# Optimization experiments

Hardware: AMD Instinct MI355X
Metric: run time of the kernel (lower is better)

## Reference

```python
import jax, jax.numpy as jnp
import numpy as np

H = 128
NH = 8  # num attention heads


def _ln(x, g, b, eps=1e-5):
    m = x.mean(-1, keepdims=True)
    v = ((x - m) ** 2).mean(-1, keepdims=True)
    return (x - m) / jnp.sqrt(v + eps) * g + b


def _mha(q_in, kv_in, Wqkv, bqkv, Wo, bo):
    # torch nn.MultiheadAttention with packed in_proj, batch=1, eval (no dropout)
    h = q_in.shape[-1]
    hd = h // NH
    Wq, Wk, Wv = Wqkv[:h], Wqkv[h:2 * h], Wqkv[2 * h:]
    bq, bk, bv = bqkv[:h], bqkv[h:2 * h], bqkv[2 * h:]
    q = (q_in @ Wq.T + bq).reshape(-1, NH, hd).transpose(1, 0, 2)   # [nh, Nq, hd]
    k = (kv_in @ Wk.T + bk).reshape(-1, NH, hd).transpose(1, 0, 2)  # [nh, Nk, hd]
    v = (kv_in @ Wv.T + bv).reshape(-1, NH, hd).transpose(1, 0, 2)
    scores = jnp.einsum('hqd,hkd->hqk', q, k) / jnp.sqrt(jnp.asarray(hd, q.dtype))
    attn = jax.nn.softmax(scores, axis=-1)
    out = jnp.einsum('hqk,hkd->hqd', attn, v)                       # [nh, Nq, hd]
    out = out.transpose(1, 0, 2).reshape(-1, h)
    return out @ Wo.T + bo


def setup_inputs() -> dict:
    key = jax.random.key(0)
    ks = jax.random.split(key, 32)
    s = 0.05
    d = {
        'ligand_features': jax.random.normal(ks[0], (512, 128), jnp.float32),
        'pocket_features': jax.random.normal(ks[1], (1024, 128), jnp.float32),
        'ligand_coords': jax.random.uniform(ks[2], (512, 3), jnp.float32) * 20.0,
        'pocket_coords': jax.random.uniform(ks[3], (1024, 3), jnp.float32) * 20.0,
        # projections
        'Wl': jax.random.normal(ks[4], (H, 128), jnp.float32) * s,
        'bl': jnp.zeros((H,), jnp.float32),
        'Wp': jax.random.normal(ks[5], (H, 128), jnp.float32) * s,
        'bp': jnp.zeros((H,), jnp.float32),
        # distance encoder: 1 -> h/4 -> h/2 -> h
        'Wd1': jax.random.normal(ks[6], (H // 4, 1), jnp.float32) * s,
        'bd1': jnp.zeros((H // 4,), jnp.float32),
        'Wd2': jax.random.normal(ks[7], (H // 2, H // 4), jnp.float32) * s,
        'bd2': jnp.zeros((H // 2,), jnp.float32),
        'Wd3': jax.random.normal(ks[8], (H, H // 2), jnp.float32) * s,
        'bd3': jnp.zeros((H,), jnp.float32),
        # gates
        'Wgl': jax.random.normal(ks[9], (H, 2 * H), jnp.float32) * s,
        'bgl': jnp.zeros((H,), jnp.float32),
        'Wgp': jax.random.normal(ks[10], (H, 2 * H), jnp.float32) * s,
        'bgp': jnp.zeros((H,), jnp.float32),
        # shared cross-attention (packed qkv like torch)
        'Wqkv': jax.random.normal(ks[11], (3 * H, H), jnp.float32) * s,
        'bqkv': jnp.zeros((3 * H,), jnp.float32),
        'Wo': jax.random.normal(ks[12], (H, H), jnp.float32) * s,
        'bo': jnp.zeros((H,), jnp.float32),
        # layer norms
        'g_l': jnp.ones((H,), jnp.float32),
        'be_l': jnp.zeros((H,), jnp.float32),
        'g_p': jnp.ones((H,), jnp.float32),
        'be_p': jnp.zeros((H,), jnp.float32),
    }
    return d


def reference(ligand_features, pocket_features, ligand_coords, pocket_coords,
              Wl, bl, Wp, bp, Wd1, bd1, Wd2, bd2, Wd3, bd3,
              Wgl, bgl, Wgp, bgp, Wqkv, bqkv, Wo, bo,
              g_l, be_l, g_p, be_p):
    lig = ligand_features @ Wl.T + bl   # [Nl, H]
    poc = pocket_features @ Wp.T + bp   # [Np, H]

    # pairwise distances [Nl, Np]
    diff = ligand_coords[:, None, :] - pocket_coords[None, :, :]
    dist = jnp.sqrt(jnp.sum(diff * diff, axis=-1))

    # distance encoder MLP applied elementwise -> [Nl, Np, H]
    e = jax.nn.relu(dist[..., None] @ Wd1.T + bd1)
    e = jax.nn.relu(e @ Wd2.T + bd2)
    enc = e @ Wd3.T + bd3
    m = enc.mean(axis=-1)               # [Nl, Np]

    # ligand enhancement: softmax over pocket axis
    sw_l = jax.nn.softmax(-m, axis=-1)          # [Nl, Np]
    agg_l = sw_l @ poc                          # [Nl, H]
    gate_l = jax.nn.sigmoid(jnp.concatenate([lig, agg_l], axis=-1) @ Wgl.T + bgl)
    lig_enh = gate_l * lig + (1.0 - gate_l) * agg_l

    # pocket enhancement: transposed encoding, softmax over ligand axis
    sw_p = jax.nn.softmax(-m.T, axis=-1)        # [Np, Nl]
    agg_p = sw_p @ lig                          # [Np, H]
    gate_p = jax.nn.sigmoid(jnp.concatenate([poc, agg_p], axis=-1) @ Wgp.T + bgp)
    poc_enh = gate_p * poc + (1.0 - gate_p) * agg_p

    lig_att = _mha(lig_enh, poc_enh, Wqkv, bqkv, Wo, bo)
    poc_att = _mha(poc_enh, lig_enh, Wqkv, bqkv, Wo, bo)

    lig_fused = _ln(lig_enh + lig_att, g_l, be_l)
    poc_fused = _ln(poc_enh + poc_att, g_p, be_p)
    return (lig_fused, poc_fused)
```

## Files before the change

kernel.cpp:

```cpp
#include <hip/hip_runtime.h>
#include <hip/hip_cooperative_groups.h>
#include <math.h>

namespace cg = cooperative_groups;

#define NL 512
#define NP 1024
#define HDIM 128

#define TAB_N 8192
#define DMAX 34.65f

#define M_OFF    128
#define WLT_OFF  (M_OFF)
#define WPT_OFF  (M_OFF + 16384)
#define WQT_OFF  (M_OFF + 32768)
#define WOT_OFF  (M_OFF + 81920)
#define WGLT_OFF (M_OFF + 98304)
#define WGPT_OFF (M_OFF + 131072)
#define TAB_OFF  (M_OFF + 163840)
#define LIG_OFF  (M_OFF + NL*NP)
#define POC_OFF  (LIG_OFF + NL*HDIM)
#define LENH_OFF (POC_OFF + NP*HDIM)
#define PENH_OFF (LENH_OFF + NL*HDIM)
#define QKVL_OFF (PENH_OFF + NP*HDIM)
#define QKVP_OFF (QKVL_OFF + NL*384)
#define PARTL_OFF (QKVP_OFF + NP*384)
#define PARTP_OFF (PARTL_OFF + 512*8*8*18)

__device__ __forceinline__ float dot4f(float4 a, float4 b){
  return fmaf(a.x,b.x, fmaf(a.y,b.y, fmaf(a.z,b.z, a.w*b.w)));
}

template<int PER>
__device__ __forceinline__ void agg_task(int t, int r0,
                                         const float* __restrict__ myC,
                                         const float* __restrict__ otC,
                                         const float* __restrict__ otherFeat,
                                         const float* __restrict__ tab,
                                         float* __restrict__ smem,
                                         float* __restrict__ aggDst)
{
  const int n = PER * 256;
  float*  w     = smem;
  float4* part4 = (float4*)(smem + 4096);
  float*  redm  = smem + 6144;
  float*  sgm   = smem + 6152;
  float*  sinv  = smem + 6154;

  int rr = t >> 8, u = t & 255;
  int lane = t & 63, wv = t >> 6;
  int row = r0 + rr;
  const float inv_h = (float)(TAB_N - 1) / DMAX;

  float cx = myC[row*3+0], cy = myC[row*3+1], cz = myC[row*3+2];

  float xs[PER];
  float lmax = -1e30f;
  #pragma unroll
  for (int k = 0; k < PER; k++){
    int j = u + (k << 8);
    float ox = otC[j*3+0], oy = otC[j*3+1], oz = otC[j*3+2];
    float dx = cx-ox, dy = cy-oy, dz = cz-oz;
    float d = sqrtf(fmaf(dx,dx, fmaf(dy,dy, dz*dz)));
    float xf = d * inv_h;
    int i0 = (int)xf;
    i0 = (i0 > TAB_N-2) ? (TAB_N-2) : i0;
    float f = xf - (float)i0;
    float v0 = tab[i0], v1 = tab[i0+1];
    xs[k] = -fmaf(f, v1 - v0, v0);
    lmax = fmaxf(lmax, xs[k]);
  }
  float v = lmax;
  #pragma unroll
  for (int off = 32; off; off >>= 1) v = fmaxf(v, __shfl_down(v, off));
  if (lane == 0) redm[wv] = v;
  __syncthreads();
  if (t < 2) sgm[t] = fmaxf(fmaxf(redm[t*4+0], redm[t*4+1]), fmaxf(redm[t*4+2], redm[t*4+3]));
  __syncthreads();
  float gm = sgm[rr];
  float lsum = 0.f;
  #pragma unroll
  for (int k = 0; k < PER; k++){
    float e = __expf(xs[k] - gm);
    w[rr*n + u + (k << 8)] = e;
    lsum += e;
  }
  v = lsum;
  #pragma unroll
  for (int off = 32; off; off >>= 1) v += __shfl_down(v, off);
  if (lane == 0) redm[wv] = v;
  __syncthreads();
  if (t < 2) sinv[t] = 1.0f / ((redm[t*4+0] + redm[t*4+1]) + (redm[t*4+2] + redm[t*4+3]));
  __syncthreads();

  {
    int jg = t >> 6;
    int r  = (t >> 5) & 1;
    int c4 = t & 31;
    const int per2 = n >> 3;
    int jb0 = jg * per2;
    const float4* of4 = (const float4*)otherFeat;
    const float* wR = w + r*n;
    float4 acc = {0,0,0,0};
    #pragma unroll 4
    for (int jj = 0; jj < per2; jj++){
      int j = jb0 + jj;
      float4 f = of4[(size_t)j*32 + c4];
      float ww = wR[j];
      acc.x = fmaf(ww, f.x, acc.x); acc.y = fmaf(ww, f.y, acc.y);
      acc.z = fmaf(ww, f.z, acc.z); acc.w = fmaf(ww, f.w, acc.w);
    }
    part4[(jg*2 + r)*32 + c4] = acc;
  }
  __syncthreads();
  #pragma unroll
  for (int s2 = 4; s2 >= 1; s2 >>= 1){
    if (t < s2*64){
      int g2 = t >> 6, rem = t & 63;
      float4 a = part4[g2*64 + rem], bb = part4[(g2+s2)*64 + rem];
      a.x += bb.x; a.y += bb.y; a.z += bb.z; a.w += bb.w;
      part4[g2*64 + rem] = a;
    }
    __syncthreads();
  }
  if (t < 256) aggDst[t] = ((const float*)part4)[t] * sinv[t >> 7];
  __syncthreads();
}

__global__ __launch_bounds__(512, 2) void fused_all(
  const float* __restrict__ lf, const float* __restrict__ pf,
  const float* __restrict__ lc, const float* __restrict__ pc,
  const float* __restrict__ Wl, const float* __restrict__ bl,
  const float* __restrict__ Wp, const float* __restrict__ bp,
  const float* __restrict__ Wd1, const float* __restrict__ bd1,
  const float* __restrict__ Wd2, const float* __restrict__ bd2,
  const float* __restrict__ Wd3, const float* __restrict__ bd3,
  const float* __restrict__ Wgl, const float* __restrict__ bgl,
  const float* __restrict__ Wgp, const float* __restrict__ bgp,
  const float* __restrict__ Wqkv, const float* __restrict__ bqkv,
  const float* __restrict__ Wo, const float* __restrict__ bo,
  const float* __restrict__ g_l, const float* __restrict__ be_l,
  const float* __restrict__ g_p, const float* __restrict__ be_p,
  float* __restrict__ ws, float* __restrict__ out)
{
  cg::grid_group grd = cg::this_grid();
  const int b = blockIdx.x;
  const int t = threadIdx.x;

  __shared__ __align__(16) float smem[16384];

  float* WlT   = ws + WLT_OFF;
  float* WpT   = ws + WPT_OFF;
  float* WqkvT = ws + WQT_OFF;
  float* WoT   = ws + WOT_OFF;
  float* WglT  = ws + WGLT_OFF;
  float* WgpT  = ws + WGPT_OFF;
  float* tab   = ws + TAB_OFF;
  float* lig   = ws + LIG_OFF;
  float* poc   = ws + POC_OFF;
  float* lenh  = ws + LENH_OFF;
  float* penh  = ws + PENH_OFF;
  float* qkvl  = ws + QKVL_OFF;
  float* qkvp  = ws + QKVP_OFF;
  float* partL = ws + PARTL_OFF;
  float* partP = ws + PARTP_OFF;

  {
    int e = b*512 + t;
    if (e < 16384){
      int o = e >> 7, k = e & 127;
      WlT[k*128 + o] = Wl[e];
    } else if (e < 32768){
      int loc = e - 16384, o = loc >> 7, k = loc & 127;
      WpT[k*128 + o] = Wp[loc];
    }
    if (e < 49152){
      int o = e >> 7, k = e & 127;
      WqkvT[k*384 + o] = Wqkv[e];
    } else if (e < 65536){
      int loc = e - 49152, o = loc >> 7, k = loc & 127;
      WoT[k*128 + o] = Wo[loc];
    } else if (e < 98304){
      int loc = e - 65536, o = loc >> 8, k = loc & 255;
      WglT[k*128 + o] = Wgl[loc];
    } else {
      int loc = e - 98304, o = loc >> 8, k = loc & 255;
      WgpT[k*128 + o] = Wgp[loc];
    }

    if (b >= 240){
      float* sWd1  = smem;
      float* sbd1  = smem + 32;
      float* sbd2  = smem + 64;
      float* swd3m = smem + 128;
      float* sWd2  = smem + 256;
      if (t < 64){
        float ssum = 0.f;
        #pragma unroll 8
        for (int i = 0; i < 128; i++) ssum += Wd3[i*64 + t];
        swd3m[t] = ssum * (1.f/128.f);
      } else if (t == 64){
        float ssum = 0.f;
        for (int i = 0; i < 128; i++) ssum += bd3[i];
        smem[192] = ssum * (1.f/128.f);
      } else if (t >= 128 && t < 160){ sWd1[t-128] = Wd1[t-128]; sbd1[t-128] = bd1[t-128]; }
      else if (t >= 160 && t < 224){ sbd2[t-160] = bd2[t-160]; }
      for (int k = t; k < 2048; k += 512) sWd2[k] = Wd2[k];
      __syncthreads();

      int idx = (b - 240)*512 + t;
      float d = (float)idx * (DMAX / (float)(TAB_N - 1));
      float4 e1q[8];
      const float4* w1q = (const float4*)sWd1;
      const float4* b1q = (const float4*)sbd1;
      #pragma unroll
      for (int k4 = 0; k4 < 8; k4++){
        float4 w = w1q[k4], bb = b1q[k4];
        float4 ev;
        ev.x = fmaxf(fmaf(d, w.x, bb.x), 0.f);
        ev.y = fmaxf(fmaf(d, w.y, bb.y), 0.f);
        ev.z = fmaxf(fmaf(d, w.z, bb.z), 0.f);
        ev.w = fmaxf(fmaf(d, w.w, bb.w), 0.f);
        e1q[k4] = ev;
      }
      float mv = smem[192];
      #pragma unroll 4
      for (int j2 = 0; j2 < 64; j2++){
        const float4* wrow = (const float4*)(sWd2 + j2*32);
        float a0 = 0.f, a1 = 0.f, a2 = 0.f, a3 = 0.f;
        #pragma unroll
        for (int k4 = 0; k4 < 8; k4++){
          float4 w = wrow[k4], ev = e1q[k4];
          a0 = fmaf(w.x, ev.x, a0);
          a1 = fmaf(w.y, ev.y, a1);
          a2 = fmaf(w.z, ev.z, a2);
          a3 = fmaf(w.w, ev.w, a3);
        }
        float e2v = fmaxf(sbd2[j2] + ((a0+a1)+(a2+a3)), 0.f);
        mv = fmaf(swd3m[j2], e2v, mv);
      }
      tab[idx] = mv;
    }
  }
  grd.sync();

  {
    int sub = t >> 8, st = t & 255;
    int nit = (b < 128) ? 2 : 1;
    for (int it = 0; it < nit; it++){
      int s = b*2 + sub + it*512;
      bool isLig = (s < 256);
      int r0 = isLig ? s*2 : (s - 256)*2;
      const float* in  = (isLig ? lf : pf) + (size_t)r0*HDIM;
      const float* WT  = isLig ? WlT : WpT;
      const float* bia = isLig ? bl : bp;
      float* o = (isLig ? lig : poc) + (size_t)r0*HDIM;
      float* sx = smem + sub*256;
      __syncthreads();
      sx[st] = in[st];
      __syncthreads();
      int r = st >> 7, col = st & 127;
      const float* xr = sx + r*HDIM;
      float acc = bia[col];
      #pragma unroll 8
      for (int k = 0; k < 128; k++) acc = fmaf(WT[k*128 + col], xr[k], acc);
      o[r*HDIM + col] = acc;
    }
  }
  grd.sync();

  {
    float* AGG = smem + 14336;
    agg_task<4>(t, 2*b,     lc, pc, poc, tab, smem, AGG);
    agg_task<2>(t, 4*b,     pc, lc, lig, tab, smem, AGG + 256);
    agg_task<2>(t, 4*b + 2, pc, lc, lig, tab, smem, AGG + 512);

    float* sx    = smem;
    float* se    = smem + 128;
    float* gpart = smem + 256;
    for (int i = 0; i < 6; i++){
      bool isLig = (i < 2);
      int row = isLig ? (2*b + i) : (4*b + (i - 2));
      const float* xsrc = (isLig ? lig : poc) + (size_t)row*HDIM;
      const float* arow = AGG + i*128;
      __syncthreads();
      if (t < 128) sx[t] = xsrc[t];
      __syncthreads();
      {
        int col = t & 127, kg = t >> 7;
        const float* WT = isLig ? WglT : WgpT;
        const float* inb = (kg < 2) ? sx : (arow - 128);
        int k0 = kg*64;
        float acc = 0.f;
        #pragma unroll 8
        for (int kk = 0; kk < 64; kk++){
          int k = k0 + kk;
          acc = fmaf(WT[(size_t)k*128 + col], inb[k], acc);
        }
        gpart[kg*128 + col] = acc;
      }
      __syncthreads();
      if (t < 128){
        const float* bg = isLig ? bgl : bgp;
        float g = bg[t] + ((gpart[t] + gpart[128+t]) + (gpart[256+t] + gpart[384+t]));
        g = 1.0f / (1.0f + __expf(-g));
        float xv = sx[t], av = arow[t];
        float enh = fmaf(g, xv - av, av);
        se[t] = enh;
        float* dst = isLig ? (lenh + (size_t)row*HDIM) : (penh + (size_t)row*HDIM);
        dst[t] = enh;
      }
      __syncthreads();
      if (t < 384){
        float acc = bqkv[t];
        #pragma unroll 8
        for (int k = 0; k < 128; k++) acc = fmaf(WqkvT[(size_t)k*384 + t], se[k], acc);
        float* q = (isLig ? qkvl : qkvp) + (size_t)row*384;
        q[t] = acc;
      }
    }
  }
  grd.sync();

  {
    for (int it = 0; it < 2; it++){
      const float* qsrc; const float* kvsrc; int qt, slice; bool isLig;
      if (it == 0){ isLig = true;  qt = b >> 3; slice = b & 7; qsrc = qkvl; kvsrc = qkvp; }
      else        { isLig = false; qt = b >> 2; slice = b & 3; qsrc = qkvp; kvsrc = qkvl; }
      int g = t >> 6, tt = t & 63;
      int h = tt >> 3, qp = tt & 7;
      int j0 = slice*128 + g*16;
      int hx = h & 3;

      const float4* qA = (const float4*)(qsrc + (size_t)(qt*16+qp)*384 + h*16);
      const float4* qB = (const float4*)(qsrc + (size_t)(qt*16+qp+8)*384 + h*16);
      float4 a0 = qA[0], a1 = qA[1], a2 = qA[2], a3 = qA[3];
      float4 b0 = qB[0], b1 = qB[1], b2 = qB[2], b3 = qB[3];
      float mA = -1e30f, lA = 0.f, mB = -1e30f, lB = 0.f;
      float4 OA0={0,0,0,0}, OA1={0,0,0,0}, OA2={0,0,0,0}, OA3={0,0,0,0};
      float4 OB0={0,0,0,0}, OB1={0,0,0,0}, OB2={0,0,0,0}, OB3={0,0,0,0};

      float* myKV = smem + g*2048;

      for (int tile = 0; tile < 2; tile++){
        int jbase = j0 + tile*8;
        __syncthreads();
        #pragma unroll
        for (int nn = 0; nn < 8; nn++){
          int v4 = tt + nn*64;
          int jj = v4 >> 6, c4 = v4 & 63;
          int c4s = (c4 & 60) | ((c4 ^ (c4 >> 2)) & 3);
          ((float4*)myKV)[jj*64 + c4s] = *(const float4*)(kvsrc + (size_t)(jbase+jj)*384 + 128 + c4*4);
        }
        __syncthreads();
        float sA[8], sB[8];
        #pragma unroll
        for (int jj = 0; jj < 8; jj++){
          const float4* kb = ((const float4*)myKV) + jj*64 + h*4;
          float4 k0 = kb[0^hx], k1 = kb[1^hx], k2 = kb[2^hx], k3 = kb[3^hx];
          sA[jj] = (dot4f(a0,k0) + dot4f(a1,k1) + dot4f(a2,k2) + dot4f(a3,k3)) * 0.25f;
          sB[jj] = (dot4f(b0,k0) + dot4f(b1,k1) + dot4f(b2,k2) + dot4f(b3,k3)) * 0.25f;
        }
        float mtA = sA[0], mtB = sB[0];
        #pragma unroll
        for (int jj = 1; jj < 8; jj++){ mtA = fmaxf(mtA, sA[jj]); mtB = fmaxf(mtB, sB[jj]); }
        float mnA = fmaxf(mA, mtA), mnB = fmaxf(mB, mtB);
        float cA = __expf(mA - mnA), cB = __expf(mB - mnB);
        lA *= cA; lB *= cB;
        OA0.x*=cA; OA0.y*=cA; OA0.z*=cA; OA0.w*=cA;
        OA1.x*=cA; OA1.y*=cA; OA1.z*=cA; OA1.w*=cA;
        OA2.x*=cA; OA2.y*=cA; OA2.z*=cA; OA2.w*=cA;
        OA3.x*=cA; OA3.y*=cA; OA3.z*=cA; OA3.w*=cA;
        OB0.x*=cB; OB0.y*=cB; OB0.z*=cB; OB0.w*=cB;
        OB1.x*=cB; OB1.y*=cB; OB1.z*=cB; OB1.w*=cB;
        OB2.x*=cB; OB2.y*=cB; OB2.z*=cB; OB2.w*=cB;
        OB3.x*=cB; OB3.y*=cB; OB3.z*=cB; OB3.w*=cB;
        #pragma unroll
        for (int jj = 0; jj < 8; jj++){
          float pA = __expf(sA[jj] - mnA);
          float pB = __expf(sB[jj] - mnB);
          lA += pA; lB += pB;
          const float4* vb = ((const float4*)myKV) + jj*64 + 32 + h*4;
          float4 v0 = vb[0^hx], v1 = vb[1^hx], v2 = vb[2^hx], v3 = vb[3^hx];
          OA0.x = fmaf(pA, v0.x, OA0.x); OA0.y = fmaf(pA, v0.y, OA0.y);
          OA0.z = fmaf(pA, v0.z, OA0.z); OA0.w = fmaf(pA, v0.w, OA0.w);
          OA1.x = fmaf(pA, v1.x, OA1.x); OA1.y = fmaf(pA, v1.y, OA1.y);
          OA1.z = fmaf(pA, v1.z, OA1.z); OA1.w = fmaf(pA, v1.w, OA1.w);
          OA2.x = fmaf(pA, v2.x, OA2.x); OA2.y = fmaf(pA, v2.y, OA2.y);
          OA2.z = fmaf(pA, v2.z, OA2.z); OA2.w = fmaf(pA, v2.w, OA2.w);
          OA3.x = fmaf(pA, v3.x, OA3.x); OA3.y = fmaf(pA, v3.y, OA3.y);
          OA3.z = fmaf(pA, v3.z, OA3.z); OA3.w = fmaf(pA, v3.w, OA3.w);
          OB0.x = fmaf(pB, v0.x, OB0.x); OB0.y = fmaf(pB, v0.y, OB0.y);
          OB0.z = fmaf(pB, v0.z, OB0.z); OB0.w = fmaf(pB, v0.w, OB0.w);
          OB1.x = fmaf(pB, v1.x, OB1.x); OB1.y = fmaf(pB, v1.y, OB1.y);
          OB1.z = fmaf(pB, v1.z, OB1.z); OB1.w = fmaf(pB, v1.w, OB1.w);
          OB2.x = fmaf(pB, v2.x, OB2.x); OB2.y = fmaf(pB, v2.y, OB2.y);
          OB2.z = fmaf(pB, v2.z, OB2.z); OB2.w = fmaf(pB, v2.w, OB2.w);
          OB3.x = fmaf(pB, v3.x, OB3.x); OB3.y = fmaf(pB, v3.y, OB3.y);
          OB3.z = fmaf(pB, v3.z, OB3.z); OB3.w = fmaf(pB, v3.w, OB3.w);
        }
        mA = mnA; mB = mnB;
      }

      __syncthreads();
      if (g > 0){
        float* bA = smem + (size_t)((g-1)*128 + tt*2)*18;
        bA[0]=mA; bA[1]=lA;
        bA[2]=OA0.x; bA[3]=OA0.y; bA[4]=OA0.z; bA[5]=OA0.w;
        bA[6]=OA1.x; bA[7]=OA1.y; bA[8]=OA1.z; bA[9]=OA1.w;
        bA[10]=OA2.x; bA[11]=OA2.y; bA[12]=OA2.z; bA[13]=OA2.w;
        bA[14]=OA3.x; bA[15]=OA3.y; bA[16]=OA3.z; bA[17]=OA3.w;
        float* bB = bA + 18;
        bB[0]=mB; bB[1]=lB;
        bB[2]=OB0.x; bB[3]=OB0.y; bB[4]=OB0.z; bB[5]=OB0.w;
        bB[6]=OB1.x; bB[7]=OB1.y; bB[8]=OB1.z; bB[9]=OB1.w;
        bB[10]=OB2.x; bB[11]=OB2.y; bB[12]=OB2.z; bB[13]=OB2.w;
        bB[14]=OB3.x; bB[15]=OB3.y; bB[16]=OB3.z; bB[17]=OB3.w;
      }
      __syncthreads();
      if (g == 0){
        float M = mA, L = lA;
        float O[16] = {OA0.x,OA0.y,OA0.z,OA0.w, OA1.x,OA1.y,OA1.z,OA1.w,
                       OA2.x,OA2.y,OA2.z,OA2.w, OA3.x,OA3.y,OA3.z,OA3.w};
        #pragma unroll
        for (int gg = 1; gg < 8; gg++){
          const float* br = smem + (size_t)((gg-1)*128 + tt*2)*18;
          float m1 = br[0], l1 = br[1];
          float Mn = fmaxf(M, m1);
          float e0 = __expf(M - Mn), e1 = __expf(m1 - Mn);
          L = L*e0 + l1*e1;
          #pragma unroll
          for (int k = 0; k < 16; k++) O[k] = O[k]*e0 + br[2+k]*e1;
          M = Mn;
        }
        int rowA = qt*16 + qp;
        float* dst = isLig ? (partL + ((size_t)(rowA*8 + h)*8 + slice)*18)
                           : (partP + ((size_t)(rowA*8 + h)*4 + slice)*18);
        dst[0] = M; dst[1] = L;
        #pragma unroll
        for (int k = 0; k < 16; k++) dst[2+k] = O[k];
        M = mB; L = lB;
        float Ob[16] = {OB0.x,OB0.y,OB0.z,OB0.w, OB1.x,OB1.y,OB1.z,OB1.w,
                        OB2.x,OB2.y,OB2.z,OB2.w, OB3.x,OB3.y,OB3.z,OB3.w};
        #pragma unroll
        for (int gg = 1; gg < 8; gg++){
          const float* br = smem + (size_t)((gg-1)*128 + tt*2)*18 + 18;
          float m1 = br[0], l1 = br[1];
          float Mn = fmaxf(M, m1);
          float e0 = __expf(M - Mn), e1 = __expf(m1 - Mn);
          L = L*e0 + l1*e1;
          #pragma unroll
          for (int k = 0; k < 16; k++) Ob[k] = Ob[k]*e0 + br[2+k]*e1;
          M = Mn;
        }
        int rowB = qt*16 + qp + 8;
        float* dstB = isLig ? (partL + ((size_t)(rowB*8 + h)*8 + slice)*18)
                            : (partP + ((size_t)(rowB*8 + h)*4 + slice)*18);
        dstB[0] = M; dstB[1] = L;
        #pragma unroll
        for (int k = 0; k < 16; k++) dstB[2+k] = Ob[k];
      }
    }
  }
  grd.sync();

  {
    int sub = t >> 8, st = t & 255;
    int nit = (b < 128) ? 2 : 1;
    for (int it = 0; it < nit; it++){
      int s = b*2 + sub + it*512;
      int r0 = s*2;
      int r = st >> 7, c = st & 127;
      int gr = r0 + r;
      int hh = c >> 4, cc = c & 15;
      int ns; const float* base;
      if (gr < NL){ ns = 8; base = partL + ((size_t)(gr*8 + hh))*8*18; }
      else        { ns = 4; base = partP + ((size_t)((gr-NL)*8 + hh))*4*18; }
      float M = -1e30f;
      for (int sl = 0; sl < ns; sl++) M = fmaxf(M, base[sl*18]);
      float Lsum = 0.f, Osum = 0.f;
      for (int sl = 0; sl < ns; sl++){
        float e = __expf(base[sl*18] - M);
        Lsum = fmaf(e, base[sl*18+1], Lsum);
        Osum = fmaf(e, base[sl*18+2+cc], Osum);
      }
      float* sAtt = smem + sub*256;
      float* sred = smem + 512 + sub*16;
      __syncthreads();
      sAtt[st] = Osum / Lsum;
      __syncthreads();
      float o = bo[c];
      const float* sA = sAtt + r*HDIM;
      #pragma unroll 8
      for (int k = 0; k < 128; k++) o = fmaf(WoT[k*128 + c], sA[k], o);
      const float* enh = (gr < NL) ? (lenh + (size_t)gr*HDIM) : (penh + (size_t)(gr-NL)*HDIM);
      float x = enh[c] + o;
      int wid = st >> 6;
      float v = x;
      #pragma unroll
      for (int off = 32; off; off >>= 1) v += __shfl_down(v, off);
      if ((st & 63) == 0) sred[wid] = v;
      __syncthreads();
      float mu = (sred[2*r] + sred[2*r+1]) * (1.f/128.f);
      float dx = x - mu;
      v = dx*dx;
      #pragma unroll
      for (int off = 32; off; off >>= 1) v += __shfl_down(v, off);
      if ((st & 63) == 0) sred[4 + wid] = v;
      __syncthreads();
      float var = (sred[4 + 2*r] + sred[4 + 2*r+1]) * (1.f/128.f);
      float y = dx * rsqrtf(var + 1e-5f);
      if (gr < NL) y = fmaf(y, g_l[c], be_l[c]);
      else         y = fmaf(y, g_p[c], be_p[c]);
      out[(size_t)gr*HDIM + c] = y;
    }
  }
}

__device__ __forceinline__ void tpose(const float* __restrict__ src, float* __restrict__ dst,
                                      int O, int K, int blk0, int t){
  int e0 = blk0*1024 + t*4;
  #pragma unroll
  for (int i = 0; i < 4; i++){
    int e = e0 + i;
    int o = e / K, k = e - o*K;
    dst[(size_t)k*O + o] = src[(size_t)o*K + k];
  }
}
__global__ __launch_bounds__(256) void prep_all(const float* __restrict__ Wl, const float* __restrict__ Wp,
                                                const float* __restrict__ Wqkv, const float* __restrict__ Wo,
                                                const float* __restrict__ Wgl, const float* __restrict__ Wgp,
                                                const float* __restrict__ Wd1, const float* __restrict__ bd1,
                                                const float* __restrict__ Wd2, const float* __restrict__ bd2,
                                                const float* __restrict__ Wd3, const float* __restrict__ bd3,
                                                float* __restrict__ ws){
  int b = blockIdx.x, t = threadIdx.x;
  if (b < 160){
    if      (b < 16)  tpose(Wl,   ws + WLT_OFF,  128, 128, b,       t);
    else if (b < 32)  tpose(Wp,   ws + WPT_OFF,  128, 128, b - 16,  t);
    else if (b < 80)  tpose(Wqkv, ws + WQT_OFF,  384, 128, b - 32,  t);
    else if (b < 96)  tpose(Wo,   ws + WOT_OFF,  128, 128, b - 80,  t);
    else if (b < 128) tpose(Wgl,  ws + WGLT_OFF, 128, 256, b - 96,  t);
    else              tpose(Wgp,  ws + WGPT_OFF, 128, 256, b - 128, t);
    return;
  }
  float* tab = ws + TAB_OFF;
  __shared__ float sWd1[32], sbd1[32], sWd2[2048], sbd2[64], swd3m[64];
  __shared__ float sbd3m;
  int idx = (b - 160) * 256 + t;
  if (t < 64){
    float s = 0.f;
    #pragma unroll 8
    for (int i = 0; i < 128; i++) s += Wd3[i*64 + t];
    swd3m[t] = s * (1.f/128.f);
  } else if (t == 64){
    float s = 0.f;
    for (int i = 0; i < 128; i++) s += bd3[i];
    sbd3m = s * (1.f/128.f);
  } else if (t >= 128 && t < 160){ sWd1[t-128] = Wd1[t-128]; sbd1[t-128] = bd1[t-128]; }
  else if (t >= 160 && t < 224){ sbd2[t-160] = bd2[t-160]; }
  for (int k = t; k < 2048; k += 256) sWd2[k] = Wd2[k];
  __syncthreads();

  float d = (float)idx * (DMAX / (float)(TAB_N - 1));
  float4 e1q[8];
  const float4* w1q = (const float4*)sWd1;
  const float4* b1q = (const float4*)sbd1;
  #pragma unroll
  for (int k4 = 0; k4 < 8; k4++){
    float4 w = w1q[k4], bb = b1q[k4];
    float4 e;
// ... 350 lines not shown
  int b = blockIdx.x, t = threadIdx.x;
  int r0 = b*2;
  int r = t >> 7, c = t & 127;
  int gr = r0 + r;
  int h = c >> 4, cc = c & 15;
  int ns; const float* base;
  if (gr < NL){ ns = 8; base = partL + ((size_t)(gr*8 + h))*8*18; }
  else        { ns = 4; base = partP + ((size_t)((gr-NL)*8 + h))*4*18; }
  float M = -1e30f;
  for (int s = 0; s < ns; s++) M = fmaxf(M, base[s*18]);
  float Lsum = 0.f, Osum = 0.f;
  for (int s = 0; s < ns; s++){
    float e = __expf(base[s*18] - M);
    Lsum = fmaf(e, base[s*18+1], Lsum);
    Osum = fmaf(e, base[s*18+2+cc], Osum);
  }
  __shared__ float sAtt[2*HDIM];
  sAtt[t] = Osum / Lsum;
  __syncthreads();
  float o = bo[c];
  const float* sA = sAtt + r*HDIM;
  #pragma unroll 8
  for (int k = 0; k < 128; k++) o = fmaf(WoT[k*128 + c], sA[k], o);
  const float* enh = (gr < NL) ? (lenh + (size_t)gr*HDIM) : (penh + (size_t)(gr-NL)*HDIM);
  float x = enh[c] + o;
  __shared__ float sred[8];
  int wid = t >> 6;
  float v = x;
  #pragma unroll
  for (int off = 32; off; off >>= 1) v += __shfl_down(v, off);
  if ((t & 63) == 0) sred[wid] = v;
  __syncthreads();
  float mu = (sred[2*r] + sred[2*r+1]) * (1.f/128.f);
  float dx = x - mu;
  v = dx*dx;
  #pragma unroll
  for (int off = 32; off; off >>= 1) v += __shfl_down(v, off);
  if ((t & 63) == 0) sred[4 + wid] = v;
  __syncthreads();
  float var = (sred[4 + 2*r] + sred[4 + 2*r+1]) * (1.f/128.f);
  float y = dx * rsqrtf(var + 1e-5f);
  if (gr < NL) y = fmaf(y, g_l[c], be_l[c]);
  else         y = fmaf(y, g_p[c], be_p[c]);
  out[(size_t)gr*HDIM + c] = y;
}

extern "C" void kernel_launch(void* const* d_in, const int* in_sizes, int n_in,
                              void* d_out, int out_size, void* d_ws, size_t ws_size,
                              hipStream_t stream){
  const float* lf   = (const float*)d_in[0];
  const float* pf   = (const float*)d_in[1];
  const float* lc   = (const float*)d_in[2];
  const float* pc   = (const float*)d_in[3];
  const float* Wl   = (const float*)d_in[4];
  const float* bl   = (const float*)d_in[5];
  const float* Wp   = (const float*)d_in[6];
  const float* bp   = (const float*)d_in[7];
  const float* Wd1  = (const float*)d_in[8];
  const float* bd1  = (const float*)d_in[9];
  const float* Wd2  = (const float*)d_in[10];
  const float* bd2  = (const float*)d_in[11];
  const float* Wd3  = (const float*)d_in[12];
  const float* bd3  = (const float*)d_in[13];
  const float* Wgl  = (const float*)d_in[14];
  const float* bgl  = (const float*)d_in[15];
  const float* Wgp  = (const float*)d_in[16];
  const float* bgp  = (const float*)d_in[17];
  const float* Wqkv = (const float*)d_in[18];
  const float* bqkv = (const float*)d_in[19];
  const float* Wo   = (const float*)d_in[20];
  const float* bo   = (const float*)d_in[21];
  const float* g_l  = (const float*)d_in[22];
  const float* be_l = (const float*)d_in[23];
  const float* g_p  = (const float*)d_in[24];
  const float* be_p = (const float*)d_in[25];

  float* ws  = (float*)d_ws;
  float* out = (float*)d_out;

  static int coop_ok = -1;
  if (coop_ok < 0){
    int nb = 0;
    hipError_t qe = hipOccupancyMaxActiveBlocksPerMultiprocessor(&nb, (const void*)fused_all, 512, 0);
    coop_ok = (qe == hipSuccess && nb >= 1) ? 1 : 0;
  }

  if (coop_ok == 1){
    void* args[] = { (void*)&lf, (void*)&pf, (void*)&lc, (void*)&pc,
                     (void*)&Wl, (void*)&bl, (void*)&Wp, (void*)&bp,
                     (void*)&Wd1, (void*)&bd1, (void*)&Wd2, (void*)&bd2,
                     (void*)&Wd3, (void*)&bd3, (void*)&Wgl, (void*)&bgl,
                     (void*)&Wgp, (void*)&bgp, (void*)&Wqkv, (void*)&bqkv,
                     (void*)&Wo, (void*)&bo, (void*)&g_l, (void*)&be_l,
                     (void*)&g_p, (void*)&be_p, (void*)&ws, (void*)&out };
    hipError_t err = hipLaunchCooperativeKernel((const void*)fused_all,
                                                dim3(256), dim3(512), args, 0, stream);
    if (err == hipSuccess) return;
    coop_ok = 0;
  }

  float* lig   = ws + LIG_OFF;
  float* poc   = ws + POC_OFF;
  float* lenh  = ws + LENH_OFF;
  float* penh  = ws + PENH_OFF;
  float* qkvl  = ws + QKVL_OFF;
  float* qkvp  = ws + QKVP_OFF;
  float* partL = ws + PARTL_OFF;
  float* partP = ws + PARTP_OFF;
  float* tab   = ws + TAB_OFF;

  prep_all<<<192, 256, 0, stream>>>(Wl, Wp, Wqkv, Wo, Wgl, Wgp, Wd1, bd1, Wd2, bd2, Wd3, bd3, ws);
  proj_kernel<<<NL/2 + NP/2, 256, 0, stream>>>(lf, pf, ws + WLT_OFF, bl, ws + WPT_OFF, bp, lig, poc);
  agg_gate_fused<<<NL/2 + NP/2, 512, 0, stream>>>(lc, pc, tab, lig, poc,
                                                  ws + WGLT_OFF, bgl, ws + WGPT_OFF, bgp,
                                                  ws + WQT_OFF, bqkv,
                                                  lenh, penh, qkvl, qkvp);
  attn_part<<<512, 256, 0, stream>>>(qkvl, qkvp, partL, partP);
  merge_ln<<<NL/2 + NP/2, 256, 0, stream>>>(partL, partP, lenh, penh, ws + WOT_OFF, bo,
                                            g_l, be_l, g_p, be_p, out);
}
```

Before: 195.3 us.

## Double cooperative grid to 512 blocks and split per-block work in half

Launches the cooperative fused kernel with 512 blocks instead of 256, two per CU on a 256-CU part. Each phase is reassigned so a block handles half as much work: one ligand row and two pocket rows in the aggregation phase, and one attention tile instead of two. The aggregation helper is reworked to process one row per 512-thread block, and the weight-transpose and table-build ranges are remapped to the larger grid. The aim is more resident waves for latency hiding and fewer serial loops per block, at the cost of costlier grid-wide syncs across more blocks and a stricter occupancy check that falls back to the multi-kernel path if two blocks per CU cannot co-reside.

Result: no change. 195.1 us (-0.1%).

```diff
diff --git a/kernel.cpp b/kernel.cpp
--- a/kernel.cpp
+++ b/kernel.cpp
@@ -32,34 +32,30 @@
   return fmaf(a.x,b.x, fmaf(a.y,b.y, fmaf(a.z,b.z, a.w*b.w)));
 }
 
-template<int PER>
-__device__ __forceinline__ void agg_task(int t, int r0,
-                                         const float* __restrict__ myC,
-                                         const float* __restrict__ otC,
-                                         const float* __restrict__ otherFeat,
-                                         const float* __restrict__ tab,
-                                         float* __restrict__ smem,
-                                         float* __restrict__ aggDst)
+template<int PERT>
+__device__ __forceinline__ void agg_row(int t, int row,
+                                        const float* __restrict__ myC,
+                                        const float* __restrict__ otC,
+                                        const float* __restrict__ otherFeat,
+                                        const float* __restrict__ tab,
+                                        float* __restrict__ smem,
+                                        float* __restrict__ aggDst)
 {
-  const int n = PER * 256;
+  const int n = PERT * 512;
   float*  w     = smem;
-  float4* part4 = (float4*)(smem + 4096);
-  float*  redm  = smem + 6144;
-  float*  sgm   = smem + 6152;
-  float*  sinv  = smem + 6154;
-
-  int rr = t >> 8, u = t & 255;
+  float4* part4 = (float4*)(smem + 1024);
+  float*  redm  = smem + 3072;
+
   int lane = t & 63, wv = t >> 6;
-  int row = r0 + rr;
   const float inv_h = (float)(TAB_N - 1) / DMAX;
 
   float cx = myC[row*3+0], cy = myC[row*3+1], cz = myC[row*3+2];
 
-  float xs[PER];
+  float xs[PERT];
   float lmax = -1e30f;
   #pragma unroll
-  for (int k = 0; k < PER; k++){
-    int j = u + (k << 8);
+  for (int k = 0; k < PERT; k++){
+    int j = t + (k << 9);
     float ox = otC[j*3+0], oy = otC[j*3+1], oz = otC[j*3+2];
     float dx = cx-ox, dy = cy-oy, dz = cz-oz;
     float d = sqrtf(fmaf(dx,dx, fmaf(dy,dy, dz*dz)));
@@ -76,14 +72,19 @@
   for (int off = 32; off; off >>= 1) v = fmaxf(v, __shfl_down(v, off));
   if (lane == 0) redm[wv] = v;
   __syncthreads();
-  if (t < 2) sgm[t] = fmaxf(fmaxf(redm[t*4+0], redm[t*4+1]), fmaxf(redm[t*4+2], redm[t*4+3]));
-  __syncthreads();
-  float gm = sgm[rr];
+  if (t == 0){
+    float m = redm[0];
+    #pragma unroll
+    for (int i = 1; i < 8; i++) m = fmaxf(m, redm[i]);
+    redm[8] = m;
+  }
+  __syncthreads();
+  float gm = redm[8];
   float lsum = 0.f;
   #pragma unroll
-  for (int k = 0; k < PER; k++){
+  for (int k = 0; k < PERT; k++){
     float e = __expf(xs[k] - gm);
-    w[rr*n + u + (k << 8)] = e;
+    w[t + (k << 9)] = e;
     lsum += e;
   }
   v = lsum;
@@ -91,40 +92,44 @@
   for (int off = 32; off; off >>= 1) v += __shfl_down(v, off);
   if (lane == 0) redm[wv] = v;
   __syncthreads();
-  if (t < 2) sinv[t] = 1.0f / ((redm[t*4+0] + redm[t*4+1]) + (redm[t*4+2] + redm[t*4+3]));
+  if (t == 0){
+    float s = 0.f;
+    #pragma unroll
+    for (int i = 0; i < 8; i++) s += redm[i];
+    redm[9] = 1.0f / s;
+  }
   __syncthreads();
 
   {
-    int jg = t >> 6;
-    int r  = (t >> 5) & 1;
+    int jg = t >> 5;
     int c4 = t & 31;
-    const int per2 = n >> 3;
+    const int per2 = n >> 4;
     int jb0 = jg * per2;
     const float4* of4 = (const float4*)otherFeat;
-    const float* wR = w + r*n;
     float4 acc = {0,0,0,0};
     #pragma unroll 4
     for (int jj = 0; jj < per2; jj++){
       int j = jb0 + jj;
       float4 f = of4[(size_t)j*32 + c4];
-      float ww = wR[j];
+      float ww = w[j];
       acc.x = fmaf(ww, f.x, acc.x); acc.y = fmaf(ww, f.y, acc.y);
       acc.z = fmaf(ww, f.z, acc.z); acc.w = fmaf(ww, f.w, acc.w);
     }
-    part4[(jg*2 + r)*32 + c4] = acc;
-  }
-  __syncthreads();
-  #pragma unroll
-  for (int s2 = 4; s2 >= 1; s2 >>= 1){
-    if (t < s2*64){
-      int g2 = t >> 6, rem = t & 63;
-      float4 a = part4[g2*64 + rem], bb = part4[(g2+s2)*64 + rem];
+    part4[jg*32 + c4] = acc;
+  }
+  __syncthreads();
+  #pragma unroll
+  for (int s2 = 8; s2 >= 1; s2 >>= 1){
+    if (t < s2*32){
+      int g2 = t >> 5, rem = t & 31;
+      float4 a = part4[g2*32 + rem], bb = part4[(g2+s2)*32 + rem];
       a.x += bb.x; a.y += bb.y; a.z += bb.z; a.w += bb.w;
-      part4[g2*64 + rem] = a;
+      part4[g2*32 + rem] = a;
     }
     __syncthreads();
   }
-  if (t < 256) aggDst[t] = ((const float*)part4)[t] * sinv[t >> 7];
+  float sinv = redm[9];
+  if (t < 128) aggDst[t] = ((const float*)part4)[t] * sinv;
   __syncthreads();
 }
 
@@ -174,22 +179,21 @@
     } else if (e < 32768){
       int loc = e - 16384, o = loc >> 7, k = loc & 127;
       WpT[k*128 + o] = Wp[loc];
-    }
-    if (e < 49152){
-      int o = e >> 7, k = e & 127;
-      WqkvT[k*384 + o] = Wqkv[e];
-    } else if (e < 65536){
-      int loc = e - 49152, o = loc >> 7, k = loc & 127;
+    } else if (e < 81920){
+      int loc = e - 32768, o = loc >> 7, k = loc & 127;
+      WqkvT[k*384 + o] = Wqkv[loc];
+    } else if (e < 98304){
+      int loc = e - 81920, o = loc >> 7, k = loc & 127;
       WoT[k*128 + o] = Wo[loc];
-    } else if (e < 98304){
-      int loc = e - 65536, o = loc >> 8, k = loc & 255;
+    } else if (e < 131072){
+      int loc = e - 98304, o = loc >> 8, k = loc & 255;
       WglT[k*128 + o] = Wgl[loc];
-    } else {
-      int loc = e - 98304, o = loc >> 8, k = loc & 255;
+    } else if (e < 163840){
+      int loc = e - 131072, o = loc >> 8, k = loc & 255;
       WgpT[k*128 + o] = Wgp[loc];
     }
 
-    if (b >= 240){
+    if (b >= 496){
       float* sWd1  = smem;
       float* sbd1  = smem + 32;
       float* sbd2  = smem + 64;
@@ -209,7 +213,7 @@
       for (int k = t; k < 2048; k += 512) sWd2[k] = Wd2[k];
       __syncthreads();
 
-      int idx = (b - 240)*512 + t;
+      int idx = (b - 496)*512 + t;
       float d = (float)idx * (DMAX / (float)(TAB_N - 1));
       float4 e1q[8];
       const float4* w1q = (const float4*)sWd1;
@@ -247,9 +251,8 @@
 
   {
     int sub = t >> 8, st = t & 255;
-    int nit = (b < 128) ? 2 : 1;
-    for (int it = 0; it < nit; it++){
-      int s = b*2 + sub + it*512;
+    int s = b*2 + sub;
+    if (s < 768){
       bool isLig = (s < 256);
       int r0 = isLig ? s*2 : (s - 256)*2;
       const float* in  = (isLig ? lf : pf) + (size_t)r0*HDIM;
@@ -257,7 +260,6 @@
       const float* bia = isLig ? bl : bp;
       float* o = (isLig ? lig : poc) + (size_t)r0*HDIM;
       float* sx = smem + sub*256;
-      __syncthreads();
       sx[st] = in[st];
       __syncthreads();
       int r = st >> 7, col = st & 127;
@@ -271,17 +273,17 @@
   grd.sync();
 
   {
-    float* AGG = smem + 14336;
-    agg_task<4>(t, 2*b,     lc, pc, poc, tab, smem, AGG);
-    agg_task<2>(t, 4*b,     pc, lc, lig, tab, smem, AGG + 256);
-    agg_task<2>(t, 4*b + 2, pc, lc, lig, tab, smem, AGG + 512);
-
-    float* sx    = smem;
-    float* se    = smem + 128;
-    float* gpart = smem + 256;
-    for (int i = 0; i < 6; i++){
-      bool isLig = (i < 2);
-      int row = isLig ? (2*b + i) : (4*b + (i - 2));
+    float* AGG = smem + 3104;
+    agg_row<2>(t, b,      lc, pc, poc, tab, smem, AGG);
+    agg_row<1>(t, 2*b,    pc, lc, lig, tab, smem, AGG + 128);
+    agg_row<1>(t, 2*b+1,  pc, lc, lig, tab, smem, AGG + 256);
+
+    float* sx    = smem + 4096;
+    float* se    = smem + 4224;
+    float* gpart = smem + 4352;
+    for (int i = 0; i < 3; i++){
+      bool isLig = (i == 0);
+      int row = isLig ? b : (2*b + (i - 1));
       const float* xsrc = (isLig ? lig : poc) + (size_t)row*HDIM;
       const float* arow = AGG + i*128;
       __syncthreads();
@@ -324,152 +326,149 @@
   grd.sync();
 
   {
-    for (int it = 0; it < 2; it++){
-      const float* qsrc; const float* kvsrc; int qt, slice; bool isLig;
-      if (it == 0){ isLig = true;  qt = b >> 3; slice = b & 7; qsrc = qkvl; kvsrc = qkvp; }
-      else        { isLig = false; qt = b >> 2; slice = b & 3; qsrc = qkvp; kvsrc = qkvl; }
-      int g = t >> 6, tt = t & 63;
-      int h = tt >> 3, qp = tt & 7;
-      int j0 = slice*128 + g*16;
-      int hx = h & 3;
-
-      const float4* qA = (const float4*)(qsrc + (size_t)(qt*16+qp)*384 + h*16);
-      const float4* qB = (const float4*)(qsrc + (size_t)(qt*16+qp+8)*384 + h*16);
-      float4 a0 = qA[0], a1 = qA[1], a2 = qA[2], a3 = qA[3];
-      float4 b0 = qB[0], b1 = qB[1], b2 = qB[2], b3 = qB[3];
-      float mA = -1e30f, lA = 0.f, mB = -1e30f, lB = 0.f;
-      float4 OA0={0,0,0,0}, OA1={0,0,0,0}, OA2={0,0,0,0}, OA3={0,0,0,0};
-      float4 OB0={0,0,0,0}, OB1={0,0,0,0}, OB2={0,0,0,0}, OB3={0,0,0,0};
-
-      float* myKV = smem + g*2048;
-
-      for (int tile = 0; tile < 2; tile++){
-        int jbase = j0 + tile*8;
-        __syncthreads();
+    const float* qsrc; const float* kvsrc; int qt, slice; bool isLig;
+    if (b < 256){ isLig = true;  qt = b >> 3; slice = b & 7; qsrc = qkvl; kvsrc = qkvp; }
+    else { int b2 = b - 256; isLig = false; qt = b2 >> 2; slice = b2 & 3; qsrc = qkvp; kvsrc = qkvl; }
+    int g = t >> 6, tt = t & 63;
+    int h = tt >> 3, qp = tt & 7;
+    int j0 = slice*128 + g*16;
+    int hx = h & 3;
+
+    const float4* qA = (const float4*)(qsrc + (size_t)(qt*16+qp)*384 + h*16);
+    const float4* qB = (const float4*)(qsrc + (size_t)(qt*16+qp+8)*384 + h*16);
+    float4 a0 = qA[0], a1 = qA[1], a2 = qA[2], a3 = qA[3];
+    float4 b0 = qB[0], b1 = qB[1], b2 = qB[2], b3 = qB[3];
+    float mA = -1e30f, lA = 0.f, mB = -1e30f, lB = 0.f;
+    float4 OA0={0,0,0,0}, OA1={0,0,0,0}, OA2={0,0,0,0}, OA3={0,0,0,0};
+    float4 OB0={0,0,0,0}, OB1={0,0,0,0}, OB2={0,0,0,0}, OB3={0,0,0,0};
+
+    float* myKV = smem + g*2048;
+
+    for (int tile = 0; tile < 2; tile++){
+      int jbase = j0 + tile*8;
+      __syncthreads();
+      #pragma unroll
+      for (int nn = 0; nn < 8; nn++){
+        int v4 = tt + nn*64;
+        int jj = v4 >> 6, c4 = v4 & 63;
+        int c4s = (c4 & 60) | ((c4 ^ (c4 >> 2)) & 3);
+        ((float4*)myKV)[jj*64 + c4s] = *(const float4*)(kvsrc + (size_t)(jbase+jj)*384 + 128 + c4*4);
+      }
+      __syncthreads();
+      float sA[8], sB[8];
+      #pragma unroll
+      for (int jj = 0; jj < 8; jj++){
+        const float4* kb = ((const float4*)myKV) + jj*64 + h*4;
+        float4 k0 = kb[0^hx], k1 = kb[1^hx], k2 = kb[2^hx], k3 = kb[3^hx];
+        sA[jj] = (dot4f(a0,k0) + dot4f(a1,k1) + dot4f(a2,k2) + dot4f(a3,k3)) * 0.25f;
+        sB[jj] = (dot4f(b0,k0) + dot4f(b1,k1) + dot4f(b2,k2) + dot4f(b3,k3)) * 0.25f;
+      }
+      float mtA = sA[0], mtB = sB[0];
+      #pragma unroll
+      for (int jj = 1; jj < 8; jj++){ mtA = fmaxf(mtA, sA[jj]); mtB = fmaxf(mtB, sB[jj]); }
+      float mnA = fmaxf(mA, mtA), mnB = fmaxf(mB, mtB);
+      float cA = __expf(mA - mnA), cB = __expf(mB - mnB);
+      lA *= cA; lB *= cB;
+      OA0.x*=cA; OA0.y*=cA; OA0.z*=cA; OA0.w*=cA;
+      OA1.x*=cA; OA1.y*=cA; OA1.z*=cA; OA1.w*=cA;
+      OA2.x*=cA; OA2.y*=cA; OA2.z*=cA; OA2.w*=cA;
+      OA3.x*=cA; OA3.y*=cA; OA3.z*=cA; OA3.w*=cA;
+      OB0.x*=cB; OB0.y*=cB; OB0.z*=cB; OB0.w*=cB;
+      OB1.x*=cB; OB1.y*=cB; OB1.z*=cB; OB1.w*=cB;
+      OB2.x*=cB; OB2.y*=cB; OB2.z*=cB; OB2.w*=cB;
+      OB3.x*=cB; OB3.y*=cB; OB3.z*=cB; OB3.w*=cB;
+      #pragma unroll
+      for (int jj = 0; jj < 8; jj++){
+        float pA = __expf(sA[jj] - mnA);
+        float pB = __expf(sB[jj] - mnB);
+        lA += pA; lB += pB;
+        const float4* vb = ((const float4*)myKV) + jj*64 + 32 + h*4;
+        float4 v0 = vb[0^hx], v1 = vb[1^hx], v2 = vb[2^hx], v3 = vb[3^hx];
+        OA0.x = fmaf(pA, v0.x, OA0.x); OA0.y = fmaf(pA, v0.y, OA0.y);
+        OA0.z = fmaf(pA, v0.z, OA0.z); OA0.w = fmaf(pA, v0.w, OA0.w);
+        OA1.x = fmaf(pA, v1.x, OA1.x); OA1.y = fmaf(pA, v1.y, OA1.y);
+        OA1.z = fmaf(pA, v1.z, OA1.z); OA1.w = fmaf(pA, v1.w, OA1.w);
+        OA2.x = fmaf(pA, v2.x, OA2.x); OA2.y = fmaf(pA, v2.y, OA2.y);
+        OA2.z = fmaf(pA, v2.z, OA2.z); OA2.w = fmaf(pA, v2.w, OA2.w);
+        OA3.x = fmaf(pA, v3.x, OA3.x); OA3.y = fmaf(pA, v3.y, OA3.y);
+        OA3.z = fmaf(pA, v3.z, OA3.z); OA3.w = fmaf(pA, v3.w, OA3.w);
+        OB0.x = fmaf(pB, v0.x, OB0.x); OB0.y = fmaf(pB, v0.y, OB0.y);
+        OB0.z = fmaf(pB, v0.z, OB0.z); OB0.w = fmaf(pB, v0.w, OB0.w);
+        OB1.x = fmaf(pB, v1.x, OB1.x); OB1.y = fmaf(pB, v1.y, OB1.y);
+        OB1.z = fmaf(pB, v1.z, OB1.z); OB1.w = fmaf(pB, v1.w, OB1.w);
+        OB2.x = fmaf(pB, v2.x, OB2.x); OB2.y = fmaf(pB, v2.y, OB2.y);
+        OB2.z = fmaf(pB, v2.z, OB2.z); OB2.w = fmaf(pB, v2.w, OB2.w);
+        OB3.x = fmaf(pB, v3.x, OB3.x); OB3.y = fmaf(pB, v3.y, OB3.y);
+        OB3.z = fmaf(pB, v3.z, OB3.z); OB3.w = fmaf(pB, v3.w, OB3.w);
+      }
+      mA = mnA; mB = mnB;
+    }
+
+    __syncthreads();
+    if (g > 0){
+      float* bA = smem + (size_t)((g-1)*128 + tt*2)*18;
+      bA[0]=mA; bA[1]=lA;
+      bA[2]=OA0.x; bA[3]=OA0.y; bA[4]=OA0.z; bA[5]=OA0.w;
+      bA[6]=OA1.x; bA[7]=OA1.y; bA[8]=OA1.z; bA[9]=OA1.w;
+      bA[10]=OA2.x; bA[11]=OA2.y; bA[12]=OA2.z; bA[13]=OA2.w;
+      bA[14]=OA3.x; bA[15]=OA3.y; bA[16]=OA3.z; bA[17]=OA3.w;
+      float* bB = bA + 18;
+      bB[0]=mB; bB[1]=lB;
+      bB[2]=OB0.x; bB[3]=OB0.y; bB[4]=OB0.z; bB[5]=OB0.w;
+      bB[6]=OB1.x; bB[7]=OB1.y; bB[8]=OB1.z; bB[9]=OB1.w;
+      bB[10]=OB2.x; bB[11]=OB2.y; bB[12]=OB2.z; bB[13]=OB2.w;
+      bB[14]=OB3.x; bB[15]=OB3.y; bB[16]=OB3.z; bB[17]=OB3.w;
+    }
+    __syncthreads();
+    if (g == 0){
+      float M = mA, L = lA;
+      float O[16] = {OA0.x,OA0.y,OA0.z,OA0.w, OA1.x,OA1.y,OA1.z,OA1.w,
+                     OA2.x,OA2.y,OA2.z,OA2.w, OA3.x,OA3.y,OA3.z,OA3.w};
+      #pragma unroll
+      for (int gg = 1; gg < 8; gg++){
+        const float* br = smem + (size_t)((gg-1)*128 + tt*2)*18;
+        float m1 = br[0], l1 = br[1];
+        float Mn = fmaxf(M, m1);
+        float e0 = __expf(M - Mn), e1 = __expf(m1 - Mn);
+        L = L*e0 + l1*e1;
         #pragma unroll
-        for (int nn = 0; nn < 8; nn++){
-          int v4 = tt + nn*64;
-          int jj = v4 >> 6, c4 = v4 & 63;
-          int c4s = (c4 & 60) | ((c4 ^ (c4 >> 2)) & 3);
-          ((float4*)myKV)[jj*64 + c4s] = *(const float4*)(kvsrc + (size_t)(jbase+jj)*384 + 128 + c4*4);
-        }
-        __syncthreads();
-        float sA[8], sB[8];
+        for (int k = 0; k < 16; k++) O[k] = O[k]*e0 + br[2+k]*e1;
+        M = Mn;
+      }
+      int rowA = qt*16 + qp;
+      float* dst = isLig ? (partL + ((size_t)(rowA*8 + h)*8 + slice)*18)
+                         : (partP + ((size_t)(rowA*8 + h)*4 + slice)*18);
+      dst[0] = M; dst[1] = L;
+      #pragma unroll
+      for (int k = 0; k < 16; k++) dst[2+k] = O[k];
+      M = mB; L = lB;
+      float Ob[16] = {OB0.x,OB0.y,OB0.z,OB0.w, OB1.x,OB1.y,OB1.z,OB1.w,
+                      OB2.x,OB2.y,OB2.z,OB2.w, OB3.x,OB3.y,OB3.z,OB3.w};
+      #pragma unroll
+      for (int gg = 1; gg < 8; gg++){
+        const float* br = smem + (size_t)((gg-1)*128 + tt*2)*18 + 18;
+        float m1 = br[0], l1 = br[1];
+        float Mn = fmaxf(M, m1);
+        float e0 = __expf(M - Mn), e1 = __expf(m1 - Mn);
+        L = L*e0 + l1*e1;
         #pragma unroll
-        for (int jj = 0; jj < 8; jj++){
-          const float4* kb = ((const float4*)myKV) + jj*64 + h*4;
-          float4 k0 = kb[0^hx], k1 = kb[1^hx], k2 = kb[2^hx], k3 = kb[3^hx];
-          sA[jj] = (dot4f(a0,k0) + dot4f(a1,k1) + dot4f(a2,k2) + dot4f(a3,k3)) * 0.25f;
-          sB[jj] = (dot4f(b0,k0) + dot4f(b1,k1) + dot4f(b2,k2) + dot4f(b3,k3)) * 0.25f;
-        }
-        float mtA = sA[0], mtB = sB[0];
-        #pragma unroll
-        for (int jj = 1; jj < 8; jj++){ mtA = fmaxf(mtA, sA[jj]); mtB = fmaxf(mtB, sB[jj]); }
-        float mnA = fmaxf(mA, mtA), mnB = fmaxf(mB, mtB);
-        float cA = __expf(mA - mnA), cB = __expf(mB - mnB);
-        lA *= cA; lB *= cB;
-        OA0.x*=cA; OA0.y*=cA; OA0.z*=cA; OA0.w*=cA;
-        OA1.x*=cA; OA1.y*=cA; OA1.z*=cA; OA1.w*=cA;
-        OA2.x*=cA; OA2.y*=cA; OA2.z*=cA; OA2.w*=cA;
-        OA3.x*=cA; OA3.y*=cA; OA3.z*=cA; OA3.w*=cA;
-        OB0.x*=cB; OB0.y*=cB; OB0.z*=cB; OB0.w*=cB;
-        OB1.x*=cB; OB1.y*=cB; OB1.z*=cB; OB1.w*=cB;
-        OB2.x*=cB; OB2.y*=cB; OB2.z*=cB; OB2.w*=cB;
-        OB3.x*=cB; OB3.y*=cB; OB3.z*=cB; OB3.w*=cB;
-        #pragma unroll
-        for (int jj = 0; jj < 8; jj++){
-          float pA = __expf(sA[jj] - mnA);
-          float pB = __expf(sB[jj] - mnB);
-          lA += pA; lB += pB;
-          const float4* vb = ((const float4*)myKV) + jj*64 + 32 + h*4;
-          float4 v0 = vb[0^hx], v1 = vb[1^hx], v2 = vb[2^hx], v3 = vb[3^hx];
-          OA0.x = fmaf(pA, v0.x, OA0.x); OA0.y = fmaf(pA, v0.y, OA0.y);
-          OA0.z = fmaf(pA, v0.z, OA0.z); OA0.w = fmaf(pA, v0.w, OA0.w);
-          OA1.x = fmaf(pA, v1.x, OA1.x); OA1.y = fmaf(pA, v1.y, OA1.y);
-          OA1.z = fmaf(pA, v1.z, OA1.z); OA1.w = fmaf(pA, v1.w, OA1.w);
-          OA2.x = fmaf(pA, v2.x, OA2.x); OA2.y = fmaf(pA, v2.y, OA2.y);
-          OA2.z = fmaf(pA, v2.z, OA2.z); OA2.w = fmaf(pA, v2.w, OA2.w);
-          OA3.x = fmaf(pA, v3.x, OA3.x); OA3.y = fmaf(pA, v3.y, OA3.y);
-          OA3.z = fmaf(pA, v3.z, OA3.z); OA3.w = fmaf(pA, v3.w, OA3.w);
-          OB0.x = fmaf(pB, v0.x, OB0.x); OB0.y = fmaf(pB, v0.y, OB0.y);
-          OB0.z = fmaf(pB, v0.z, OB0.z); OB0.w = fmaf(pB, v0.w, OB0.w);
-          OB1.x = fmaf(pB, v1.x, OB1.x); OB1.y = fmaf(pB, v1.y, OB1.y);
-          OB1.z = fmaf(pB, v1.z, OB1.z); OB1.w = fmaf(pB, v1.w, OB1.w);
-          OB2.x = fmaf(pB, v2.x, OB2.x); OB2.y = fmaf(pB, v2.y, OB2.y);
-          OB2.z = fmaf(pB, v2.z, OB2.z); OB2.w = fmaf(pB, v2.w, OB2.w);
-          OB3.x = fmaf(pB, v3.x, OB3.x); OB3.y = fmaf(pB, v3.y, OB3.y);
-          OB3.z = fmaf(pB, v3.z, OB3.z); OB3.w = fmaf(pB, v3.w, OB3.w);
-        }
-        mA = mnA; mB = mnB;
-      }
-
-      __syncthreads();
-      if (g > 0){
-        float* bA = smem + (size_t)((g-1)*128 + tt*2)*18;
-        bA[0]=mA; bA[1]=lA;
-        bA[2]=OA0.x; bA[3]=OA0.y; bA[4]=OA0.z; bA[5]=OA0.w;
-        bA[6]=OA1.x; bA[7]=OA1.y; bA[8]=OA1.z; bA[9]=OA1.w;
-        bA[10]=OA2.x; bA[11]=OA2.y; bA[12]=OA2.z; bA[13]=OA2.w;
-        bA[14]=OA3.x; bA[15]=OA3.y; bA[16]=OA3.z; bA[17]=OA3.w;
-        float* bB = bA + 18;
-        bB[0]=mB; bB[1]=lB;
-        bB[2]=OB0.x; bB[3]=OB0.y; bB[4]=OB0.z; bB[5]=OB0.w;
-        bB[6]=OB1.x; bB[7]=OB1.y; bB[8]=OB1.z; bB[9]=OB1.w;
-        bB[10]=OB2.x; bB[11]=OB2.y; bB[12]=OB2.z; bB[13]=OB2.w;
-        bB[14]=OB3.x; bB[15]=OB3.y; bB[16]=OB3.z; bB[17]=OB3.w;
-      }
-      __syncthreads();
-      if (g == 0){
-        float M = mA, L = lA;
-        float O[16] = {OA0.x,OA0.y,OA0.z,OA0.w, OA1.x,OA1.y,OA1.z,OA1.w,
-                       OA2.x,OA2.y,OA2.z,OA2.w, OA3.x,OA3.y,OA3.z,OA3.w};
-        #pragma unroll
-        for (int gg = 1; gg < 8; gg++){
-          const float* br = smem + (size_t)((gg-1)*128 + tt*2)*18;
-          float m1 = br[0], l1 = br[1];
-          float Mn = fmaxf(M, m1);
-          float e0 = __expf(M - Mn), e1 = __expf(m1 - Mn);
-          L = L*e0 + l1*e1;
-          #pragma unroll
-          for (int k = 0; k < 16; k++) O[k] = O[k]*e0 + br[2+k]*e1;
-          M = Mn;
-        }
-        int rowA = qt*16 + qp;
-        float* dst = isLig ? (partL + ((size_t)(rowA*8 + h)*8 + slice)*18)
-                           : (partP + ((size_t)(rowA*8 + h)*4 + slice)*18);
-        dst[0] = M; dst[1] = L;
-        #pragma unroll
-        for (int k = 0; k < 16; k++) dst[2+k] = O[k];
-        M = mB; L = lB;
-        float Ob[16] = {OB0.x,OB0.y,OB0.z,OB0.w, OB1.x,OB1.y,OB1.z,OB1.w,
-                        OB2.x,OB2.y,OB2.z,OB2.w, OB3.x,OB3.y,OB3.z,OB3.w};
-        #pragma unroll
-        for (int gg = 1; gg < 8; gg++){
-          const float* br = smem + (size_t)((gg-1)*128 + tt*2)*18 + 18;
-          float m1 = br[0], l1 = br[1];
-          float Mn = fmaxf(M, m1);
-          float e0 = __expf(M - Mn), e1 = __expf(m1 - Mn);
-          L = L*e0 + l1*e1;
-          #pragma unroll
-          for (int k = 0; k < 16; k++) Ob[k] = Ob[k]*e0 + br[2+k]*e1;
-          M = Mn;
-        }
-        int rowB = qt*16 + qp + 8;
-        float* dstB = isLig ? (partL + ((size_t)(rowB*8 + h)*8 + slice)*18)
-                            : (partP + ((size_t)(rowB*8 + h)*4 + slice)*18);
-        dstB[0] = M; dstB[1] = L;
-        #pragma unroll
-        for (int k = 0; k < 16; k++) dstB[2+k] = Ob[k];
-      }
+        for (int k = 0; k < 16; k++) Ob[k] = Ob[k]*e0 + br[2+k]*e1;
+        M = Mn;
+      }
+      int rowB = qt*16 + qp + 8;
+      float* dstB = isLig ? (partL + ((size_t)(rowB*8 + h)*8 + slice)*18)
+                          : (partP + ((size_t)(rowB*8 + h)*4 + slice)*18);
+      dstB[0] = M; dstB[1] = L;
+      #pragma unroll
+      for (int k = 0; k < 16; k++) dstB[2+k] = Ob[k];
     }
   }
   grd.sync();
 
   {
     int sub = t >> 8, st = t & 255;
-    int nit = (b < 128) ? 2 : 1;
-    for (int it = 0; it < nit; it++){
-      int s = b*2 + sub + it*512;
+    int s = b*2 + sub;
+    if (s < 768){
       int r0 = s*2;
       int r = st >> 7, c = st & 127;
       int gr = r0 + r;
@@ -487,7 +486,6 @@
       }
       float* sAtt = smem + sub*256;
       float* sred = smem + 512 + sub*16;
-      __syncthreads();
       sAtt[st] = Osum / Lsum;
       __syncthreads();
       float o = bo[c];
@@ -1004,7 +1002,7 @@
   if (coop_ok < 0){
     int nb = 0;
     hipError_t qe = hipOccupancyMaxActiveBlocksPerMultiprocessor(&nb, (const void*)fused_all, 512, 0);
-    coop_ok = (qe == hipSuccess && nb >= 1) ? 1 : 0;
+    coop_ok = (qe == hipSuccess && nb >= 2) ? 1 : 0;
   }
 
   if (coop_ok == 1){
@@ -1016,7 +1014,7 @@
                      (void*)&Wo, (void*)&bo, (void*)&g_l, (void*)&be_l,
                      (void*)&g_p, (void*)&be_p, (void*)&ws, (void*)&out };
     hipError_t err = hipLaunchCooperativeKernel((const void*)fused_all,
-                                                dim3(256), dim3(512), args, 0, stream);
+                                                dim3(512), dim3(512), args, 0, stream);
     if (err == hipSuccess) return;
     coop_ok = 0;
   }
```
